# Optimization experiments

Hardware: AMD Instinct MI355X
Metric: run time of the kernel (lower is better)

The kernel has to match this reference:

```python
import jax, jax.numpy as jnp
import numpy as np

DN = ('NCHW', 'OIHW', 'NCHW')

def _conv(x, w, pad):
    return jax.lax.conv_general_dilated(x, w, window_strides=(1, 1),
                                        padding=[(pad, pad), (pad, pad)],
                                        dimension_numbers=DN)

def _channel_shuffle(x, perm):
    # x: [B, C, H, W]; perm: [C, H*W] per-channel spatial permutation
    B, C, H, W = x.shape
    y = jnp.take_along_axis(x.reshape(B, C, H * W), perm[None, :, :], axis=2)
    return y.reshape(B, C, H, W)

def setup_inputs() -> dict:
    key = jax.random.key(0)
    k = jax.random.split(key, 6)
    B, Cin, H, W = 32, 1024, 28, 28
    P1, P2, P3 = 256, 256, 1024
    HW = H * W
    x = jax.random.normal(k[0], (B, Cin, H, W), dtype=jnp.float32)
    w1 = jax.random.normal(k[1], (P1, Cin, 1, 1), dtype=jnp.float32) * np.sqrt(2.0 / Cin)
    wd = jax.random.normal(k[2], (P2, P1, 3, 3), dtype=jnp.float32) * np.sqrt(2.0 / (P1 * 9))
    w3 = jax.random.normal(k[3], (P3, P2, 1, 1), dtype=jnp.float32) * np.sqrt(2.0 / P2)
    perm_dconv = jax.vmap(lambda kk: jax.random.permutation(kk, HW))(
        jax.random.split(k[4], P1)).astype(jnp.int32)
    perm_res = jax.vmap(lambda kk: jax.random.permutation(kk, HW))(
        jax.random.split(k[5], Cin)).astype(jnp.int32)
    return {"x": x, "w1": w1, "wd": wd, "w3": w3,
            "perm_dconv": perm_dconv, "perm_res": perm_res}

def reference(x, w1, wd, w3, perm_dconv, perm_res):
    # conv1 (1x1) + relu
    y = jax.nn.relu(_conv(x, w1, 0))
    # Dconv_shuffle: per-channel spatial shuffle then 3x3 conv (pad=1), relu
    y = _channel_shuffle(y, perm_dconv)
    y = jax.nn.relu(_conv(y, wd, 1))
    # conv3 (1x1)
    y = _conv(y, w3, 0)
    # residual: per-channel spatially shuffled input, add, relu
    res = _channel_shuffle(x, perm_res)
    return jax.nn.relu(y + res)
```

## Files before the change

### kernel.cpp

```cpp
#include <hip/hip_runtime.h>
#include <hip/hip_bf16.h>

#define BATCH 32
#define CIN   1024
#define HW    784
#define WIMG  28
#define PADW  30
#define PADHW 900
#define P1    256
#define P2    256
#define P3    1024
#define NFLAT (BATCH * HW)

typedef __attribute__((ext_vector_type(8))) short bfrag_t;
typedef __attribute__((ext_vector_type(8))) unsigned short usvec8;
typedef __attribute__((ext_vector_type(4))) float accvec_t;

static __device__ __forceinline__ unsigned short f2bf(float f) {
    union { __hip_bfloat16 h; unsigned short u; } cv;
    cv.h = __float2bfloat16(f);
    return cv.u;
}
static __device__ __forceinline__ float bf2f(unsigned short u) {
    union { float f; unsigned int i; } cv;
    cv.i = ((unsigned int)u) << 16;
    return cv.f;
}

#define GLDS16(g, l) __builtin_amdgcn_global_load_lds(                      \
        (const __attribute__((address_space(1))) void*)(g),                 \
        (__attribute__((address_space(3))) void*)(l), 16, 0, 0)

__global__ __launch_bounds__(256) void permT_kernel(const int* __restrict__ perm,
                                                    int* __restrict__ permT) {
    int p = blockIdx.x, c = threadIdx.x;
    permT[p * P1 + c] = perm[c * HW + p];
}

__global__ __launch_bounds__(256) void pack_weights_kernel(
        const float* __restrict__ w1, const float* __restrict__ wd,
        const float* __restrict__ w3, unsigned short* __restrict__ w1b,
        unsigned short* __restrict__ wdb, unsigned short* __restrict__ w3b) {
    int i = blockIdx.x * 256 + threadIdx.x;
    if (i < 262144) w1b[i] = f2bf(w1[i]);
    int i2 = i - 262144;
    if (i2 >= 0 && i2 < 262144) w3b[i2] = f2bf(w3[i2]);
    int i3 = i - 524288;
    if (i3 >= 0 && i3 < 589824) {
        int m = i3 / 2304, rem = i3 - m * 2304;
        int k = rem / 9, r = rem - k * 9;
        wdb[((size_t)r * P2 + m) * P1 + k] = f2bf(wd[i3]);
    }
}

__global__ __launch_bounds__(256) void transpose_x_kernel(const float* __restrict__ x,
                                                          unsigned short* __restrict__ xt) {
    __shared__ unsigned short T[64 * 66];
    const int b   = blockIdx.z;
    const int c0  = blockIdx.x * 64;
    const int hw0 = blockIdx.y * 64;
    const int t = threadIdx.x;
    const int j = t & 63, i0 = t >> 6;
    const float* xb = x + ((size_t)b * CIN + c0) * HW + hw0;
    const bool jv = (hw0 + j) < HW;
#pragma unroll
    for (int ii = 0; ii < 16; ++ii) {
        int i = i0 * 16 + ii;
        float v = jv ? xb[(size_t)i * HW + j] : 0.f;
        T[i * 66 + j] = f2bf(v);
    }
    __syncthreads();
#pragma unroll
    for (int ii = 0; ii < 16; ++ii) {
        int rr = i0 * 16 + ii;
        if (hw0 + rr < HW)
            xt[((size_t)b * HW + hw0 + rr) * CIN + c0 + j] = T[j * 66 + rr];
    }
}

__global__ __launch_bounds__(256) void res_shuffle_kernel(const float* __restrict__ x,
                                                          const int* __restrict__ perm_res,
                                                          unsigned short* __restrict__ res) {
    __shared__ float Lx[8 * 788];
    const int g0 = blockIdx.x * 8;
    const int t = threadIdx.x;
#pragma unroll
    for (int it = 0; it < 7; ++it) {
        int chunk = it * 256 + t;
        if (chunk < 1568) {
            int r = chunk / 196, off = (chunk - r * 196) * 4;
            float4 v = *(const float4*)&x[(size_t)(g0 + r) * HW + off];
            *(float4*)&Lx[r * 788 + off] = v;
        }
    }
    __syncthreads();
    const int q0 = t & 63;
#pragma unroll
    for (int rp = 0; rp < 2; ++rp) {
        int r = rp * 4 + (t >> 6);
        int g = g0 + r;
        int m = g & (CIN - 1);
        const int* pr = perm_res + (size_t)m * HW;
#pragma unroll
        for (int it = 0; it < 13; ++it) {
            int q = it * 64 + q0;
            if (q < HW) {
                int pv = pr[q];
                res[(size_t)g * HW + q] = f2bf(Lx[r * 788 + pv]);
            }
        }
    }
}

__global__ __launch_bounds__(256) void shuffle_pad_kernel(const unsigned short* __restrict__ y1c,
                                                          const int* __restrict__ permT,
                                                          unsigned short* __restrict__ y1sp) {
    __shared__ unsigned short Ly[32 * 800];
    const int b  = blockIdx.x >> 3;
    const int c0 = (blockIdx.x & 7) * 32;
    const int t = threadIdx.x;
#pragma unroll
    for (int it = 0; it < 13; ++it) {
        int chunk = it * 256 + t;
        if (chunk < 3136) {
            int c = chunk / 98, off8 = (chunk - c * 98) * 8;
            usvec8 v = *(const usvec8*)&y1c[((size_t)(b * P1 + c0 + c)) * HW + off8];
            *(usvec8*)&Ly[c * 800 + off8] = v;
        }
    }
    __syncthreads();
    const int pc = t & 31, pi = t >> 5;
    unsigned short* yb = y1sp + (size_t)b * PADHW * P1 + c0 + pc;
#pragma unroll 4
    for (int it = 0; it < 98; ++it) {
        int p = it * 8 + pi;
        int pv = permT[p * P1 + c0 + pc];
        unsigned short val = Ly[pc * 800 + pv];
        int ph = p / WIMG, pw = p - ph * WIMG;
        yb[(size_t)((ph + 1) * PADW + pw + 1) * P1] = val;
    }
}


__global__ __launch_bounds__(256) void conv1_kernel(const unsigned short* __restrict__ xt,
                                                    const unsigned short* __restrict__ w1b,
                                                    unsigned short* __restrict__ y1c) {
    __shared__ __align__(16) unsigned short As[128 * 64];
    __shared__ __align__(16) unsigned short Bs[128 * 64];
    const int m0 = blockIdx.x * 128;
    const int n0 = blockIdx.y * 128;
    const int t = threadIdx.x;
    const int lane = t & 63, wave = t >> 6;
    const int l15 = lane & 15, quad = lane >> 4;
    const int wm = wave & 1, wn = wave >> 1;
    const int grow = lane >> 3;
    const int gsw  = ((lane & 7) ^ grow) << 3;
    const unsigned short* Asrc[4];
    const unsigned short* Bsrc[4];
    int ldso[4];
#pragma unroll
    for (int j = 0; j < 4; ++j) {
        int q = wave * 4 + j;
        int row = (q << 3) + grow;
        Asrc[j] = w1b + (size_t)(m0 + row) * CIN + gsw;
        Bsrc[j] = xt + (size_t)(n0 + row) * CIN + gsw;
        ldso[j] = q * 512;
    }
    const int coff0 = ((quad)     ^ (l15 & 7)) << 3;
    const int coff1 = ((quad + 4) ^ (l15 & 7)) << 3;

    accvec_t acc[4][4];
    const accvec_t zero = {0.f, 0.f, 0.f, 0.f};
#pragma unroll
    for (int i = 0; i < 4; ++i)
#pragma unroll
        for (int j = 0; j < 4; ++j) acc[i][j] = zero;

    for (int k0 = 0; k0 < CIN; k0 += 64) {
#pragma unroll
        for (int j = 0; j < 4; ++j) {
            GLDS16(Asrc[j] + k0, &As[ldso[j]]);
            GLDS16(Bsrc[j] + k0, &Bs[ldso[j]]);
        }
        __syncthreads();
        bfrag_t af[4], bfr[4];
#pragma unroll
        for (int i = 0; i < 4; ++i) {
            af[i]  = *(const bfrag_t*)&As[(wm * 64 + i * 16 + l15) * 64 + coff0];
            bfr[i] = *(const bfrag_t*)&Bs[(wn * 64 + i * 16 + l15) * 64 + coff0];
        }
#pragma unroll
        for (int im = 0; im < 4; ++im)
#pragma unroll
            for (int in = 0; in < 4; ++in)
                acc[im][in] = __builtin_amdgcn_mfma_f32_16x16x32_bf16(af[im], bfr[in], acc[im][in], 0, 0, 0);
#pragma unroll
        for (int i = 0; i < 4; ++i) {
            af[i]  = *(const bfrag_t*)&As[(wm * 64 + i * 16 + l15) * 64 + coff1];
            bfr[i] = *(const bfrag_t*)&Bs[(wn * 64 + i * 16 + l15) * 64 + coff1];
        }
#pragma unroll
        for (int im = 0; im < 4; ++im)
#pragma unroll
            for (int in = 0; in < 4; ++in)
                acc[im][in] = __builtin_amdgcn_mfma_f32_16x16x32_bf16(af[im], bfr[in], acc[im][in], 0, 0, 0);
        __syncthreads();
    }
#pragma unroll
    for (int in = 0; in < 4; ++in) {
        const int n = n0 + wn * 64 + in * 16 + l15;
        const int b = n / HW, hw = n - b * HW;
#pragma unroll
        for (int im = 0; im < 4; ++im) {
#pragma unroll
            for (int r = 0; r < 4; ++r) {
                const int m = m0 + wm * 64 + im * 16 + (quad << 2) + r;
                float v = acc[im][in][r];
                v = v > 0.f ? v : 0.f;
                y1c[((size_t)(b * P1 + m)) * HW + hw] = f2bf(v);
            }
        }
    }
}

__global__ __launch_bounds__(256) void dconv_kernel(const unsigned short* __restrict__ y1sp,
                                                    const unsigned short* __restrict__ wdb,
                                                    unsigned short* __restrict__ y2t) {
    __shared__ __align__(16) unsigned short As[128 * 64];
    __shared__ __align__(16) unsigned short Bs[128 * 64];
    const int m0 = blockIdx.x * 128;
    const int n0 = blockIdx.y * 128;
    const int t = threadIdx.x;
    const int lane = t & 63, wave = t >> 6;
    const int l15 = lane & 15, quad = lane >> 4;
    const int wm = wave & 1, wn = wave >> 1;
    const int grow = lane >> 3;
    const int gsw  = ((lane & 7) ^ grow) << 3;
    const unsigned short* Asrc[4];
    const unsigned short* Bsrc[4];
    int ldso[4];
#pragma unroll
    for (int j = 0; j < 4; ++j) {
        int q = wave * 4 + j;
        int row = (q << 3) + grow;
        Asrc[j] = wdb + (size_t)(m0 + row) * P1 + gsw;
        int n = n0 + row;
        int b = n / HW, hw = n - b * HW;
        int h = hw / WIMG, w = hw - h * WIMG;
        Bsrc[j] = y1sp + ((size_t)b * PADHW + h * PADW + w) * P1 + gsw;
        ldso[j] = q * 512;
    }
    const int coff0 = ((quad)     ^ (l15 & 7)) << 3;
    const int coff1 = ((quad + 4) ^ (l15 & 7)) << 3;

    accvec_t acc[4][4];
    const accvec_t zero = {0.f, 0.f, 0.f, 0.f};
#pragma unroll
    for (int i = 0; i < 4; ++i)
#pragma unroll
        for (int j = 0; j < 4; ++j) acc[i][j] = zero;

    for (int r = 0; r < 9; ++r) {
        const int kh = r / 3, kw = r - kh * 3;
        const size_t aoff = (size_t)r * (P1 * P2);
        const int taboff = (kh * PADW + kw) * P1;
        for (int k0 = 0; k0 < P1; k0 += 64) {
#pragma unroll
            for (int j = 0; j < 4; ++j) {
                GLDS16(Asrc[j] + aoff + k0, &As[ldso[j]]);
                GLDS16(Bsrc[j] + taboff + k0, &Bs[ldso[j]]);
            }
            __syncthreads();
            bfrag_t af[4], bfr[4];
#pragma unroll
            for (int i = 0; i < 4; ++i) {
                af[i]  = *(const bfrag_t*)&As[(wm * 64 + i * 16 + l15) * 64 + coff0];
                bfr[i] = *(const bfrag_t*)&Bs[(wn * 64 + i * 16 + l15) * 64 + coff0];
            }
#pragma unroll
            for (int im = 0; im < 4; ++im)
#pragma unroll
                for (int in = 0; in < 4; ++in)
                    acc[im][in] = __builtin_amdgcn_mfma_f32_16x16x32_bf16(bfr[in], af[im], acc[im][in], 0, 0, 0);
#pragma unroll
            for (int i = 0; i < 4; ++i) {
                af[i]  = *(const bfrag_t*)&As[(wm * 64 + i * 16 + l15) * 64 + coff1];
                bfr[i] = *(const bfrag_t*)&Bs[(wn * 64 + i * 16 + l15) * 64 + coff1];
            }
#pragma unroll
            for (int im = 0; im < 4; ++im)
#pragma unroll
                for (int in = 0; in < 4; ++in)
                    acc[im][in] = __builtin_amdgcn_mfma_f32_16x16x32_bf16(bfr[in], af[im], acc[im][in], 0, 0, 0);
            __syncthreads();
        }
    }
#pragma unroll
    for (int im = 0; im < 4; ++im) {
        const int m = m0 + wm * 64 + im * 16 + l15;
#pragma unroll
        for (int in = 0; in < 4; ++in) {
#pragma unroll
            for (int r = 0; r < 4; ++r) {
                const int n = n0 + wn * 64 + in * 16 + (quad << 2) + r;
                float v = acc[im][in][r];
                v = v > 0.f ? v : 0.f;
                y2t[(size_t)n * P2 + m] = f2bf(v);
            }
        }
    }
}

__global__ __launch_bounds__(256) void conv3_kernel(const unsigned short* __restrict__ y2t,
                                                    const unsigned short* __restrict__ w3b,
                                                    const unsigned short* __restrict__ res,
                                                    float* __restrict__ out) {
    __shared__ __align__(16) unsigned short As[128 * 32];
    __shared__ __align__(16) unsigned short Bs[128 * 32];
    const int m0 = blockIdx.x * 128;
    const int n0 = blockIdx.y * 128;
    const int t = threadIdx.x;
    const int lane = t & 63, wave = t >> 6;
    const int l15 = lane & 15, quad = lane >> 4;
    const int wm = wave & 1, wn = wave >> 1;
    const int srow = lane >> 2, c8 = (lane & 3) << 3;
    const int row0 = wave * 32 + srow, row1 = row0 + 16;

    const unsigned short* a0 = w3b + (size_t)(m0 + row0) * P2 + c8;
    const unsigned short* a1 = w3b + (size_t)(m0 + row1) * P2 + c8;
    const unsigned short* b0 = y2t + (size_t)(n0 + row0) * P2 + c8;
    const unsigned short* b1 = y2t + (size_t)(n0 + row1) * P2 + c8;
    unsigned short* Ad0 = &As[(wave * 2 + 0) * 512];
    unsigned short* Ad1 = &As[(wave * 2 + 1) * 512];
    unsigned short* Bd0 = &Bs[(wave * 2 + 0) * 512];
    unsigned short* Bd1 = &Bs[(wave * 2 + 1) * 512];

    accvec_t acc[4][4];
    const accvec_t zero = {0.f, 0.f, 0.f, 0.f};
#pragma unroll
    for (int i = 0; i < 4; ++i)
#pragma unroll
        for (int j = 0; j < 4; ++j) acc[i][j] = zero;

    for (int k0 = 0; k0 < P2; k0 += 32) {
        GLDS16(a0 + k0, Ad0);
        GLDS16(a1 + k0, Ad1);
        GLDS16(b0 + k0, Bd0);
        GLDS16(b1 + k0, Bd1);
        __syncthreads();
        bfrag_t af[4], bfr[4];
#pragma unroll
        for (int i = 0; i < 4; ++i) {
            af[i]  = *(const bfrag_t*)&As[(wm * 64 + i * 16 + l15) * 32 + (quad << 3)];
            bfr[i] = *(const bfrag_t*)&Bs[(wn * 64 + i * 16 + l15) * 32 + (quad << 3)];
        }
#pragma unroll
        for (int im = 0; im < 4; ++im)
#pragma unroll
            for (int in = 0; in < 4; ++in)
                acc[im][in] = __builtin_amdgcn_mfma_f32_16x16x32_bf16(af[im], bfr[in], acc[im][in], 0, 0, 0);
        __syncthreads();
    }
#pragma unroll
    for (int in = 0; in < 4; ++in) {
        const int n = n0 + wn * 64 + in * 16 + l15;
        const int b = n / HW, hw = n - b * HW;
#pragma unroll
        for (int im = 0; im < 4; ++im) {
#pragma unroll
            for (int r = 0; r < 4; ++r) {
                const int m = m0 + wm * 64 + im * 16 + (quad << 2) + r;
                const size_t idx = ((size_t)(b * P3 + m)) * HW + hw;
                float v = acc[im][in][r] + bf2f(res[idx]);
                v = v > 0.f ? v : 0.f;
                out[idx] = v;
            }
        }
    }
}

extern "C" void kernel_launch(void* const* d_in, const int* in_sizes, int n_in,
                              void* d_out, int out_size, void* d_ws, size_t ws_size,
                              hipStream_t stream) {
    const float* x      = (const float*)d_in[0];
    const float* w1     = (const float*)d_in[1];
    const float* wd     = (const float*)d_in[2];
    const float* w3     = (const float*)d_in[3];
    const int*   perm_d = (const int*)d_in[4];
    const int*   perm_r = (const int*)d_in[5];
    float*       out    = (float*)d_out;

    char* ws = (char*)d_ws;
    unsigned short* y1sp  = (unsigned short*)(ws + 0);
    unsigned short* y2t   = (unsigned short*)(ws + 14745600);
    int*            permT = (int*)(ws + 27590656);
    unsigned short* w1b   = (unsigned short*)(ws + 28393472);
    unsigned short* wdb   = (unsigned short*)(ws + 28917760);
    unsigned short* w3b   = (unsigned short*)(ws + 30097408);
    unsigned short* xt    = (unsigned short*)(ws + 30621696);
    unsigned short* resb  = xt;
    unsigned short* y1c   = y2t;

    hipMemsetAsync(y1sp, 0, (size_t)BATCH * PADHW * P1 * sizeof(unsigned short), stream);
    permT_kernel<<<dim3(HW), dim3(256), 0, stream>>>(perm_d, permT);
    pack_weights_kernel<<<dim3(4352), dim3(256), 0, stream>>>(w1, wd, w3, w1b, wdb, w3b);
    transpose_x_kernel<<<dim3(16, 13, BATCH), dim3(256), 0, stream>>>(x, xt);

    conv1_kernel<<<dim3(P1 / 128, NFLAT / 128), dim3(256), 0, stream>>>(xt, w1b, y1c);
    res_shuffle_kernel<<<dim3(BATCH * CIN / 8), dim3(256), 0, stream>>>(x, perm_r, resb);
    shuffle_pad_kernel<<<dim3(BATCH * 8), dim3(256), 0, stream>>>(y1c, permT, y1sp);
    dconv_kernel<<<dim3(P2 / 128, NFLAT / 128), dim3(256), 0, stream>>>(y1sp, wdb, y2t);
    conv3_kernel<<<dim3(P3 / 128, NFLAT / 128), dim3(256), 0, stream>>>(y2t, w3b, resb, out);
}
```

Before: 395.4 us.

## Fuse x transpose with residual shuffle, drop memset, remap GEMM grids, widen conv3 K-tile

Replaces the x transpose kernel with one that stages each 64-channel block of x in LDS once, then writes both the channel-last bf16 copy and the permuted residual. The separate residual pass runs only when the workspace is too small to hold both buffers. The full-buffer memset of the padded activation is replaced by zeroing only the border pixels inside shuffle_pad_kernel. The three GEMM kernels switch to a 1D grid with a remapped block order so that neighbouring blocks share N tiles. conv3 moves to 64-wide K tiles with swizzled LDS, matching conv1. Together these aim to cut redundant reads of x, memset traffic and cache misses, at the cost of a larger workspace and more code complexity.

```diff
diff --git a/kernel.cpp b/kernel.cpp
--- a/kernel.cpp
+++ b/kernel.cpp
@@ -11,6 +11,7 @@
 #define P2    256
 #define P3    1024
 #define NFLAT (BATCH * HW)
+#define NT    196
 
 typedef __attribute__((ext_vector_type(8))) short bfrag_t;
 typedef __attribute__((ext_vector_type(8))) unsigned short usvec8;
@@ -53,28 +54,37 @@
     }
 }
 
-__global__ __launch_bounds__(256) void transpose_x_kernel(const float* __restrict__ x,
-                                                          unsigned short* __restrict__ xt) {
-    __shared__ unsigned short T[64 * 66];
-    const int b   = blockIdx.z;
-    const int c0  = blockIdx.x * 64;
-    const int hw0 = blockIdx.y * 64;
-    const int t = threadIdx.x;
-    const int j = t & 63, i0 = t >> 6;
-    const float* xb = x + ((size_t)b * CIN + c0) * HW + hw0;
-    const bool jv = (hw0 + j) < HW;
-#pragma unroll
-    for (int ii = 0; ii < 16; ++ii) {
-        int i = i0 * 16 + ii;
-        float v = jv ? xb[(size_t)i * HW + j] : 0.f;
-        T[i * 66 + j] = f2bf(v);
+__global__ __launch_bounds__(512) void prep_x_kernel(const float* __restrict__ x,
+                                                     const int* __restrict__ perm_res,
+                                                     unsigned short* __restrict__ xt,
+                                                     unsigned short* __restrict__ res,
+                                                     int write_res) {
+    __shared__ unsigned short Ly[64 * 790];
+    const int b  = blockIdx.x >> 4;
+    const int c0 = (blockIdx.x & 15) * 64;
+    const int t = threadIdx.x;
+    const float* xb = x + ((size_t)(b * CIN + c0)) * HW;
+    for (int chunk = t; chunk < 12544; chunk += 512) {
+        int c = chunk / 196, f4 = (chunk - c * 196) * 4;
+        float4 v = *(const float4*)&xb[(size_t)c * HW + f4];
+        unsigned short* d = &Ly[c * 790 + f4];
+        d[0] = f2bf(v.x); d[1] = f2bf(v.y); d[2] = f2bf(v.z); d[3] = f2bf(v.w);
     }
     __syncthreads();
-#pragma unroll
-    for (int ii = 0; ii < 16; ++ii) {
-        int rr = i0 * 16 + ii;
-        if (hw0 + rr < HW)
-            xt[((size_t)b * HW + hw0 + rr) * CIN + c0 + j] = T[j * 66 + rr];
+    const int w = t >> 6, j = t & 63;
+    unsigned short* xto = xt + ((size_t)b * HW) * CIN + c0 + j;
+    const int hw1 = w * 98 + 98;
+    for (int hw = w * 98; hw < hw1; ++hw)
+        xto[(size_t)hw * CIN] = Ly[j * 790 + hw];
+    if (write_res) {
+#pragma unroll
+        for (int ci = 0; ci < 8; ++ci) {
+            int c = w * 8 + ci;
+            const int* pr = perm_res + (size_t)(c0 + c) * HW;
+            unsigned short* ro = res + ((size_t)(b * CIN + c0 + c)) * HW;
+            for (int q = j; q < HW; q += 64)
+                ro[q] = Ly[c * 790 + pr[q]];
+        }
     }
 }
 
@@ -104,10 +114,7 @@
 #pragma unroll
         for (int it = 0; it < 13; ++it) {
             int q = it * 64 + q0;
-            if (q < HW) {
-                int pv = pr[q];
-                res[(size_t)g * HW + q] = f2bf(Lx[r * 788 + pv]);
-            }
+            if (q < HW) res[(size_t)g * HW + q] = f2bf(Lx[r * 788 + pr[q]]);
         }
     }
 }
@@ -119,6 +126,16 @@
     const int b  = blockIdx.x >> 3;
     const int c0 = (blockIdx.x & 7) * 32;
     const int t = threadIdx.x;
+    unsigned short* ybase = y1sp + (size_t)b * PADHW * P1 + c0;
+    for (int idx = t; idx < 116 * 32; idx += 256) {
+        int bp = idx >> 5, c = idx & 31;
+        int pos;
+        if (bp < 30)      pos = bp;
+        else if (bp < 60) pos = 870 + (bp - 30);
+        else if (bp < 88) pos = (bp - 60 + 1) * 30;
+        else              pos = (bp - 88 + 1) * 30 + 29;
+        ybase[(size_t)pos * P1 + c] = 0;
+    }
 #pragma unroll
     for (int it = 0; it < 13; ++it) {
         int chunk = it * 256 + t;
@@ -130,7 +147,7 @@
     }
     __syncthreads();
     const int pc = t & 31, pi = t >> 5;
-    unsigned short* yb = y1sp + (size_t)b * PADHW * P1 + c0 + pc;
+    unsigned short* yb = ybase + pc;
 #pragma unroll 4
     for (int it = 0; it < 98; ++it) {
         int p = it * 8 + pi;
@@ -145,10 +162,15 @@
 __global__ __launch_bounds__(256) void conv1_kernel(const unsigned short* __restrict__ xt,
                                                     const unsigned short* __restrict__ w1b,
                                                     unsigned short* __restrict__ y1c) {
+    const int g = blockIdx.x;
+    const int rcls = g & 7, s = g >> 3;
+    const int mt = s & 1, q = s >> 1;
+    const int nt = q * 8 + rcls;
+    if (nt >= NT) return;
+    const int m0 = mt * 128, n0 = nt * 128;
+
     __shared__ __align__(16) unsigned short As[128 * 64];
     __shared__ __align__(16) unsigned short Bs[128 * 64];
-    const int m0 = blockIdx.x * 128;
-    const int n0 = blockIdx.y * 128;
     const int t = threadIdx.x;
     const int lane = t & 63, wave = t >> 6;
     const int l15 = lane & 15, quad = lane >> 4;
@@ -160,11 +182,11 @@
     int ldso[4];
 #pragma unroll
     for (int j = 0; j < 4; ++j) {
-        int q = wave * 4 + j;
-        int row = (q << 3) + grow;
+        int qq = wave * 4 + j;
+        int row = (qq << 3) + grow;
         Asrc[j] = w1b + (size_t)(m0 + row) * CIN + gsw;
         Bsrc[j] = xt + (size_t)(n0 + row) * CIN + gsw;
-        ldso[j] = q * 512;
+        ldso[j] = qq * 512;
     }
     const int coff0 = ((quad)     ^ (l15 & 7)) << 3;
     const int coff1 = ((quad + 4) ^ (l15 & 7)) << 3;
@@ -226,10 +248,15 @@
 __global__ __launch_bounds__(256) void dconv_kernel(const unsigned short* __restrict__ y1sp,
                                                     const unsigned short* __restrict__ wdb,
                                                     unsigned short* __restrict__ y2t) {
+    const int g = blockIdx.x;
+    const int rcls = g & 7, s = g >> 3;
+    const int mt = s & 1, q = s >> 1;
+    const int nt = q * 8 + rcls;
+    if (nt >= NT) return;
+    const int m0 = mt * 128, n0 = nt * 128;
+
     __shared__ __align__(16) unsigned short As[128 * 64];
     __shared__ __align__(16) unsigned short Bs[128 * 64];
-    const int m0 = blockIdx.x * 128;
-    const int n0 = blockIdx.y * 128;
     const int t = threadIdx.x;
     const int lane = t & 63, wave = t >> 6;
     const int l15 = lane & 15, quad = lane >> 4;
@@ -241,14 +268,14 @@
     int ldso[4];
 #pragma unroll
     for (int j = 0; j < 4; ++j) {
-        int q = wave * 4 + j;
-        int row = (q << 3) + grow;
+        int qq = wave * 4 + j;
+        int row = (qq << 3) + grow;
         Asrc[j] = wdb + (size_t)(m0 + row) * P1 + gsw;
         int n = n0 + row;
         int b = n / HW, hw = n - b * HW;
         int h = hw / WIMG, w = hw - h * WIMG;
         Bsrc[j] = y1sp + ((size_t)b * PADHW + h * PADW + w) * P1 + gsw;
-        ldso[j] = q * 512;
+        ldso[j] = qq * 512;
     }
     const int coff0 = ((quad)     ^ (l15 & 7)) << 3;
     const int coff1 = ((quad + 4) ^ (l15 & 7)) << 3;
@@ -315,25 +342,34 @@
                                                     const unsigned short* __restrict__ w3b,
                                                     const unsigned short* __restrict__ res,
                                                     float* __restrict__ out) {
-    __shared__ __align__(16) unsigned short As[128 * 32];
-    __shared__ __align__(16) unsigned short Bs[128 * 32];
-    const int m0 = blockIdx.x * 128;
-    const int n0 = blockIdx.y * 128;
+    const int g = blockIdx.x;
+    const int rcls = g & 7, s = g >> 3;
+    const int mt = s & 7, q = s >> 3;
+    const int nt = q * 8 + rcls;
+    if (nt >= NT) return;
+    const int m0 = mt * 128, n0 = nt * 128;
+
+    __shared__ __align__(16) unsigned short As[128 * 64];
+    __shared__ __align__(16) unsigned short Bs[128 * 64];
     const int t = threadIdx.x;
     const int lane = t & 63, wave = t >> 6;
     const int l15 = lane & 15, quad = lane >> 4;
     const int wm = wave & 1, wn = wave >> 1;
-    const int srow = lane >> 2, c8 = (lane & 3) << 3;
-    const int row0 = wave * 32 + srow, row1 = row0 + 16;
-
-    const unsigned short* a0 = w3b + (size_t)(m0 + row0) * P2 + c8;
-    const unsigned short* a1 = w3b + (size_t)(m0 + row1) * P2 + c8;
-    const unsigned short* b0 = y2t + (size_t)(n0 + row0) * P2 + c8;
-    const unsigned short* b1 = y2t + (size_t)(n0 + row1) * P2 + c8;
-    unsigned short* Ad0 = &As[(wave * 2 + 0) * 512];
-    unsigned short* Ad1 = &As[(wave * 2 + 1) * 512];
-    unsigned short* Bd0 = &Bs[(wave * 2 + 0) * 512];
-    unsigned short* Bd1 = &Bs[(wave * 2 + 1) * 512];
+    const int grow = lane >> 3;
+    const int gsw  = ((lane & 7) ^ grow) << 3;
+    const unsigned short* Asrc[4];
+    const unsigned short* Bsrc[4];
+    int ldso[4];
+#pragma unroll
+    for (int j = 0; j < 4; ++j) {
+        int qq = wave * 4 + j;
+        int row = (qq << 3) + grow;
+        Asrc[j] = w3b + (size_t)(m0 + row) * P2 + gsw;
+        Bsrc[j] = y2t + (size_t)(n0 + row) * P2 + gsw;
+        ldso[j] = qq * 512;
+    }
+    const int coff0 = ((quad)     ^ (l15 & 7)) << 3;
+    const int coff1 = ((quad + 4) ^ (l15 & 7)) << 3;
 
     accvec_t acc[4][4];
     const accvec_t zero = {0.f, 0.f, 0.f, 0.f};
@@ -342,17 +378,28 @@
 #pragma unroll
         for (int j = 0; j < 4; ++j) acc[i][j] = zero;
 
-    for (int k0 = 0; k0 < P2; k0 += 32) {
-        GLDS16(a0 + k0, Ad0);
-        GLDS16(a1 + k0, Ad1);
-        GLDS16(b0 + k0, Bd0);
-        GLDS16(b1 + k0, Bd1);
+    for (int k0 = 0; k0 < P2; k0 += 64) {
+#pragma unroll
+        for (int j = 0; j < 4; ++j) {
+            GLDS16(Asrc[j] + k0, &As[ldso[j]]);
+            GLDS16(Bsrc[j] + k0, &Bs[ldso[j]]);
+        }
         __syncthreads();
         bfrag_t af[4], bfr[4];
 #pragma unroll
         for (int i = 0; i < 4; ++i) {
-            af[i]  = *(const bfrag_t*)&As[(wm * 64 + i * 16 + l15) * 32 + (quad << 3)];
-            bfr[i] = *(const bfrag_t*)&Bs[(wn * 64 + i * 16 + l15) * 32 + (quad << 3)];
+            af[i]  = *(const bfrag_t*)&As[(wm * 64 + i * 16 + l15) * 64 + coff0];
+            bfr[i] = *(const bfrag_t*)&Bs[(wn * 64 + i * 16 + l15) * 64 + coff0];
+        }
+#pragma unroll
+        for (int im = 0; im < 4; ++im)
+#pragma unroll
+            for (int in = 0; in < 4; ++in)
+                acc[im][in] = __builtin_amdgcn_mfma_f32_16x16x32_bf16(af[im], bfr[in], acc[im][in], 0, 0, 0);
+#pragma unroll
+        for (int i = 0; i < 4; ++i) {
+            af[i]  = *(const bfrag_t*)&As[(wm * 64 + i * 16 + l15) * 64 + coff1];
+            bfr[i] = *(const bfrag_t*)&Bs[(wn * 64 + i * 16 + l15) * 64 + coff1];
         }
 #pragma unroll
         for (int im = 0; im < 4; ++im)
@@ -398,17 +445,19 @@
     unsigned short* wdb   = (unsigned short*)(ws + 28917760);
     unsigned short* w3b   = (unsigned short*)(ws + 30097408);
     unsigned short* xt    = (unsigned short*)(ws + 30621696);
-    unsigned short* resb  = xt;
     unsigned short* y1c   = y2t;
-
-    hipMemsetAsync(y1sp, 0, (size_t)BATCH * PADHW * P1 * sizeof(unsigned short), stream);
+    const size_t FUSED_WS = 82001920ULL + 51380224ULL;
+    const bool fused = ws_size >= FUSED_WS;
+    unsigned short* resb = fused ? (unsigned short*)(ws + 82001920) : xt;
+
     permT_kernel<<<dim3(HW), dim3(256), 0, stream>>>(perm_d, permT);
     pack_weights_kernel<<<dim3(4352), dim3(256), 0, stream>>>(w1, wd, w3, w1b, wdb, w3b);
-    transpose_x_kernel<<<dim3(16, 13, BATCH), dim3(256), 0, stream>>>(x, xt);
-
-    conv1_kernel<<<dim3(P1 / 128, NFLAT / 128), dim3(256), 0, stream>>>(xt, w1b, y1c);
-    res_shuffle_kernel<<<dim3(BATCH * CIN / 8), dim3(256), 0, stream>>>(x, perm_r, resb);
+    prep_x_kernel<<<dim3(512), dim3(512), 0, stream>>>(x, perm_r, xt, resb, fused ? 1 : 0);
+
+    conv1_kernel<<<dim3(400), dim3(256), 0, stream>>>(xt, w1b, y1c);
+    if (!fused)
+        res_shuffle_kernel<<<dim3(BATCH * CIN / 8), dim3(256), 0, stream>>>(x, perm_r, resb);
     shuffle_pad_kernel<<<dim3(BATCH * 8), dim3(256), 0, stream>>>(y1c, permT, y1sp);
-    dconv_kernel<<<dim3(P2 / 128, NFLAT / 128), dim3(256), 0, stream>>>(y1sp, wdb, y2t);
-    conv3_kernel<<<dim3(P3 / 128, NFLAT / 128), dim3(256), 0, stream>>>(y2t, w3b, resb, out);
-}
+    dconv_kernel<<<dim3(400), dim3(256), 0, stream>>>(y1sp, wdb, y2t);
+    conv3_kernel<<<dim3(1600), dim3(256), 0, stream>>>(y2t, w3b, resb, out);
+}
```

After: 424.6 us. +7.4%, slower.
